# Kernel tuning notes

Hardware: AMD Instinct MI355X
Metric: run time of the kernel (lower is better)

Reference implementation:

```python
import jax, jax.numpy as jnp
import numpy as np

B, V, E, D_IN, D_OUT = 8, 10000, 160000, 128, 128
BN_EPS = 1e-5


def setup_inputs() -> dict:
    key = jax.random.key(0)
    ks = jax.random.split(key, 8)
    X = jax.random.normal(ks[0], (B, V, D_IN), dtype=jnp.float32)
    edge_attr = jax.random.normal(ks[1], (B, E), dtype=jnp.float32)
    W_node = jax.random.normal(ks[2], (D_OUT, D_IN), dtype=jnp.float32) * (1.0 / np.sqrt(D_IN))
    W_edge = jax.random.normal(ks[3], (D_OUT, 1), dtype=jnp.float32)
    W_self = jax.random.normal(ks[4], (D_OUT, D_IN), dtype=jnp.float32) * (1.0 / np.sqrt(D_IN))
    b_self = jax.random.normal(ks[5], (D_OUT,), dtype=jnp.float32) * 0.01
    gamma = jnp.ones((D_OUT,), dtype=jnp.float32)
    beta = jnp.zeros((D_OUT,), dtype=jnp.float32)
    edge_index = jax.random.randint(ks[6], (E, 2), 0, V, dtype=jnp.int32)
    return {"X": X, "edge_attr": edge_attr, "W_node": W_node, "W_edge": W_edge,
            "W_self": W_self, "b_self": b_self, "gamma": gamma, "beta": beta,
            "edge_index": edge_index}


def reference(X, edge_attr, W_node, W_edge, W_self, b_self, gamma, beta, edge_index):
    src = edge_index[:, 0]  # [E]
    dst = edge_index[:, 1]  # [E]
    # self-loop linear
    H = jnp.einsum('bvf,of->bvo', X, W_self) + b_self  # [B,V,D_OUT]
    # fused gather -> per-edge message -> scatter-add
    msg = jnp.einsum('bef,of->beo', X[:, src, :], W_node)  # [B,E,D_OUT]
    msg = msg + edge_attr[:, :, None] * W_edge[:, 0][None, None, :]
    aggregated = jnp.zeros_like(H).at[:, dst, :].add(msg)
    H = H + aggregated
    # BatchNorm1d over channel dim (training mode, biased variance over B*V)
    mean = jnp.mean(H, axis=(0, 1))
    var = jnp.var(H, axis=(0, 1))
    Hn = (H - mean) * jax.lax.rsqrt(var + BN_EPS) * gamma + beta
    return jax.nn.relu(Hn)
```

## Files before the change

### kernel.cpp

```cpp
#include <hip/hip_runtime.h>

#define B_ 8
#define V_ 10000
#define E_ 160000
#define DIN 128
#define DOUT 128
#define M_ (B_*V_)
#define NINV (1.0f/80000.0f)
#define BN_EPS 1e-5f

#define WS_COUNTS  0
#define WS_SUM     10000
#define WS_SUMSQ   10128
#define WS_ROWPTR  10512
#define WS_CURSOR  20513
#define WS_SSRC    30513
#define WS_SEID    190513
#define WS_S       350513
#define WS_WPK     430516
#define WS_XBF     446900
#define WS_ABF     5566900
#define WS_ZERO_UNITS 10256

typedef __attribute__((ext_vector_type(8))) short short8;
typedef __attribute__((ext_vector_type(4))) float f32x4;

__device__ inline unsigned short f2bf(float x) {
    union { float f; unsigned u; } v; v.f = x;
    unsigned r = v.u + 0x7FFFu + ((v.u >> 16) & 1u);
    return (unsigned short)(r >> 16);
}
__device__ inline float bf2f(unsigned short u) {
    union { unsigned u; float f; } v; v.u = ((unsigned)u) << 16;
    return v.f;
}

__global__ __launch_bounds__(256) void prep_kernel(
    const float* __restrict__ X, unsigned short* __restrict__ Xbf,
    const float* __restrict__ Wself, const float* __restrict__ Wnode,
    unsigned short* __restrict__ Wpk,
    const int* __restrict__ EI, int* __restrict__ counts)
{
    const int blk = blockIdx.x;
    const int t = threadIdx.x;
    if (blk < 10000) {
        int idx = blk * 256 + t;
        float4 v = ((const float4*)X)[idx];
        ushort4 o;
        o.x = f2bf(v.x); o.y = f2bf(v.y); o.z = f2bf(v.z); o.w = f2bf(v.w);
        ((ushort4*)Xbf)[idx] = o;
    } else if (blk < 10016) {
        int g = (blk - 10000) * 256 + t;
        int pair = g >> 6;
        int lane = g & 63;
        int ks = pair >> 3;
        int nt = pair & 7;
        int o = nt * 16 + (lane & 15);
        int k = ks * 32 + (lane >> 4) * 8;
        const float* wsrc = (k < 128) ? (Wself + o * 128 + k)
                                      : (Wnode + o * 128 + (k - 128));
        unsigned short* dst = Wpk + ((size_t)pair * 64 + lane) * 8;
#pragma unroll
        for (int j = 0; j < 8; ++j) dst[j] = f2bf(wsrc[j]);
    } else {
        int e = (blk - 10016) * 256 + t;
        if (e < E_) atomicAdd(&counts[EI[2 * e + 1]], 1);
    }
}

__global__ __launch_bounds__(256) void scan_kernel(
    const int* __restrict__ counts, int* __restrict__ row_ptr,
    int* __restrict__ cursor)
{
    __shared__ int psum[256];
    const int t = threadIdx.x;
    const int base = t * 40;
    int local[40];
    int s = 0;
#pragma unroll
    for (int i = 0; i < 40; ++i) {
        int idx = base + i;
        int c = (idx < V_) ? counts[idx] : 0;
        local[i] = s;
        s += c;
    }
    psum[t] = s;
    __syncthreads();
    for (int off = 1; off < 256; off <<= 1) {
        int v = (t >= off) ? psum[t - off] : 0;
        __syncthreads();
        psum[t] += v;
        __syncthreads();
    }
    int excl = (t == 0) ? 0 : psum[t - 1];
#pragma unroll
    for (int i = 0; i < 40; ++i) {
        int idx = base + i;
        if (idx < V_) {
            int rp = excl + local[i];
            row_ptr[idx] = rp;
            cursor[idx] = rp;
        }
    }
    if (t == 255) row_ptr[V_] = psum[255];
}

__global__ __launch_bounds__(256) void bucket_kernel(
    const int* __restrict__ EI, int* __restrict__ cursor,
    int* __restrict__ ssrc, int* __restrict__ seid)
{
    int e = blockIdx.x * 256 + threadIdx.x;
    if (e < E_) {
        int src = EI[2 * e];
        int dst = EI[2 * e + 1];
        int p = atomicAdd(&cursor[dst], 1);
        ssrc[p] = src;
        seid[p] = e;
    }
}

__global__ __launch_bounds__(256) void gather_kernel(
    const unsigned short* __restrict__ Xbf, const float* __restrict__ EA,
    const int* __restrict__ row_ptr, const int* __restrict__ ssrc,
    const int* __restrict__ seid, unsigned short* __restrict__ Abf,
    float* __restrict__ S)
{
    const int b = blockIdx.x & 7;
    const int dblk = blockIdx.x >> 3;
    const int w = threadIdx.x >> 6;
    const int lane = threadIdx.x & 63;
    const int d = dblk * 4 + w;
    const int wid = b * V_ + d;
    const int k0 = row_ptr[d];
    const int k1 = row_ptr[d + 1];
    const unsigned short* Xb = Xbf + (size_t)b * V_ * DIN + lane * 2;
    const float* EAb = EA + (size_t)b * E_;
    float ax = 0.0f, ay = 0.0f;
    float ea = 0.0f;
    for (int kb = k0; kb < k1; kb += 64) {
        int cnt = min(64, k1 - kb);
        int msrc = 0;
        if (lane < cnt) {
            msrc = ssrc[kb + lane];
            ea += EAb[seid[kb + lane]];
        }
        int j = 0;
        for (; j + 4 <= cnt; j += 4) {
            int s0 = __shfl(msrc, j);
            int s1 = __shfl(msrc, j + 1);
            int s2 = __shfl(msrc, j + 2);
            int s3 = __shfl(msrc, j + 3);
            ushort2 v0 = *(const ushort2*)(Xb + (size_t)s0 * DIN);
            ushort2 v1 = *(const ushort2*)(Xb + (size_t)s1 * DIN);
            ushort2 v2 = *(const ushort2*)(Xb + (size_t)s2 * DIN);
            ushort2 v3 = *(const ushort2*)(Xb + (size_t)s3 * DIN);
            ax += bf2f(v0.x) + bf2f(v1.x) + bf2f(v2.x) + bf2f(v3.x);
            ay += bf2f(v0.y) + bf2f(v1.y) + bf2f(v2.y) + bf2f(v3.y);
        }
        for (; j < cnt; ++j) {
            int s = __shfl(msrc, j);
            ushort2 v = *(const ushort2*)(Xb + (size_t)s * DIN);
            ax += bf2f(v.x); ay += bf2f(v.y);
        }
    }
    for (int off = 32; off; off >>= 1) ea += __shfl_down(ea, off);
    if (lane == 0) S[wid] = ea;
    ushort2 o;
    o.x = f2bf(ax); o.y = f2bf(ay);
    *(ushort2*)(Abf + (size_t)wid * DIN + lane * 2) = o;
}

__global__ __launch_bounds__(256) void mfma_gemm_kernel(
    const unsigned short* __restrict__ Xbf, const unsigned short* __restrict__ Abf,
    const unsigned short* __restrict__ Wpk, const float* __restrict__ S,
    const float* __restrict__ bself, const float* __restrict__ wedge,
    float* __restrict__ H, float* __restrict__ gsum, float* __restrict__ gsumsq)
{
    __shared__ float cs[128];
    __shared__ float css[128];
    const int t = threadIdx.x;
    const int wave = t >> 6;
    const int lane = t & 63;
    const int quad = lane >> 4;
    const int ln = lane & 15;
    const int rowbase = blockIdx.x * 128 + wave * 32;
    const int m0 = rowbase + ln;
    const int m1 = rowbase + 16 + ln;

    if (t < 128) { cs[t] = 0.0f; css[t] = 0.0f; }

    f32x4 acc[2][8];
#pragma unroll
    for (int mt = 0; mt < 2; ++mt)
#pragma unroll
        for (int nt = 0; nt < 8; ++nt) acc[mt][nt] = (f32x4){0.f, 0.f, 0.f, 0.f};

    const short* X0 = (const short*)Xbf + (size_t)m0 * DIN + quad * 8;
    const short* X1 = (const short*)Xbf + (size_t)m1 * DIN + quad * 8;
    const short* A0 = (const short*)Abf + (size_t)m0 * DIN + quad * 8;
    const short* A1 = (const short*)Abf + (size_t)m1 * DIN + quad * 8;
    const short* Wl = (const short*)Wpk + lane * 8;

#pragma unroll
    for (int ks = 0; ks < 8; ++ks) {
        short8 bfr[8];
#pragma unroll
        for (int nt = 0; nt < 8; ++nt)
            bfr[nt] = *(const short8*)(Wl + (size_t)(ks * 8 + nt) * 512);
        short8 af0, af1;
        if (ks < 4) {
            af0 = *(const short8*)(X0 + ks * 32);
            af1 = *(const short8*)(X1 + ks * 32);
        } else {
            af0 = *(const short8*)(A0 + (ks - 4) * 32);
            af1 = *(const short8*)(A1 + (ks - 4) * 32);
        }
#pragma unroll
        for (int nt = 0; nt < 8; ++nt) {
            acc[0][nt] = __builtin_amdgcn_mfma_f32_16x16x32_bf16(af0, bfr[nt], acc[0][nt], 0, 0, 0);
            acc[1][nt] = __builtin_amdgcn_mfma_f32_16x16x32_bf16(af1, bfr[nt], acc[1][nt], 0, 0, 0);
        }
    }

    float bs[8], we[8];
#pragma unroll
    for (int nt = 0; nt < 8; ++nt) {
        int c = nt * 16 + ln;
        bs[nt] = bself[c];
        we[nt] = wedge[c];
    }
    float psum[8], psq[8];
#pragma unroll
    for (int nt = 0; nt < 8; ++nt) { psum[nt] = 0.0f; psq[nt] = 0.0f; }

#pragma unroll
    for (int mt = 0; mt < 2; ++mt) {
        const int rbase = rowbase + mt * 16 + quad * 4;
        float sv[4];
#pragma unroll
        for (int r = 0; r < 4; ++r) sv[r] = S[rbase + r];
#pragma unroll
        for (int r = 0; r < 4; ++r) {
            float* Hr = H + (size_t)(rbase + r) * DOUT + ln;
#pragma unroll
            for (int nt = 0; nt < 8; ++nt) {
                float h = acc[mt][nt][r] + bs[nt] + sv[r] * we[nt];
                Hr[nt * 16] = h;
                psum[nt] += h;
                psq[nt] += h * h;
            }
        }
    }
#pragma unroll
    for (int nt = 0; nt < 8; ++nt) {
        psum[nt] += __shfl_down(psum[nt], 32);
        psum[nt] += __shfl_down(psum[nt], 16);
        psq[nt] += __shfl_down(psq[nt], 32);
        psq[nt] += __shfl_down(psq[nt], 16);
    }
    __syncthreads();
    if (lane < 16) {
#pragma unroll
        for (int nt = 0; nt < 8; ++nt) {
            atomicAdd(&cs[nt * 16 + ln], psum[nt]);
            atomicAdd(&css[nt * 16 + ln], psq[nt]);
        }
    }
    __syncthreads();
    if (t < 128) {
        atomicAdd(&gsum[t], cs[t]);
        atomicAdd(&gsumsq[t], css[t]);
    }
}

__global__ __launch_bounds__(256) void norm_relu_kernel(
    float* __restrict__ H, const float* __restrict__ gsum,
    const float* __restrict__ gsumsq, const float* __restrict__ gamma,
    const float* __restrict__ beta)
{
    int idx = blockIdx.x * 256 + threadIdx.x;
    int o4 = (idx & 31) * 4;
    float4 s = *(const float4*)(gsum + o4);
    float4 q = *(const float4*)(gsumsq + o4);
    float4 g = *(const float4*)(gamma + o4);
    float4 bt = *(const float4*)(beta + o4);
    float4 sc, sh;
    {
        float m0 = s.x * NINV, m1 = s.y * NINV, m2 = s.z * NINV, m3 = s.w * NINV;
        float r0 = rsqrtf(q.x * NINV - m0 * m0 + BN_EPS);
        float r1 = rsqrtf(q.y * NINV - m1 * m1 + BN_EPS);
        float r2 = rsqrtf(q.z * NINV - m2 * m2 + BN_EPS);
        float r3 = rsqrtf(q.w * NINV - m3 * m3 + BN_EPS);
        sc.x = g.x * r0; sc.y = g.y * r1; sc.z = g.z * r2; sc.w = g.w * r3;
        sh.x = bt.x - m0 * sc.x; sh.y = bt.y - m1 * sc.y;
        sh.z = bt.z - m2 * sc.z; sh.w = bt.w - m3 * sc.w;
    }
    float4 h = ((const float4*)H)[idx];
    h.x = fmaxf(h.x * sc.x + sh.x, 0.0f);
    h.y = fmaxf(h.y * sc.y + sh.y, 0.0f);
    h.z = fmaxf(h.z * sc.z + sh.z, 0.0f);
    h.w = fmaxf(h.w * sc.w + sh.w, 0.0f);
    ((float4*)H)[idx] = h;
}

extern "C" void kernel_launch(void* const* d_in, const int* in_sizes, int n_in,
                              void* d_out, int out_size, void* d_ws, size_t ws_size,
                              hipStream_t stream)
{
    const float* X      = (const float*)d_in[0];
    const float* EA     = (const float*)d_in[1];
    const float* Wnode  = (const float*)d_in[2];
    const float* Wedge  = (const float*)d_in[3];
    const float* Wself  = (const float*)d_in[4];
    const float* bself  = (const float*)d_in[5];
    const float* gamma  = (const float*)d_in[6];
    const float* beta   = (const float*)d_in[7];
    const int*   EI     = (const int*)d_in[8];

    int*   wsI    = (int*)d_ws;
    float* wsF    = (float*)d_ws;
    int*   counts = wsI + WS_COUNTS;
    float* gsum   = wsF + WS_SUM;
    float* gsumsq = wsF + WS_SUMSQ;
    int*   rowptr = wsI + WS_ROWPTR;
    int*   cursor = wsI + WS_CURSOR;
    int*   ssrc   = wsI + WS_SSRC;
    int*   seid   = wsI + WS_SEID;
    float* S      = wsF + WS_S;
    unsigned short* Wpk = (unsigned short*)(wsI + WS_WPK);
    unsigned short* Xbf = (unsigned short*)(wsI + WS_XBF);
    unsigned short* Abf = (unsigned short*)(wsI + WS_ABF);
    float* H      = (float*)d_out;

    hipMemsetAsync(d_ws, 0, (size_t)WS_ZERO_UNITS * 4, stream);

    prep_kernel<<<10641, 256, 0, stream>>>(X, Xbf, Wself, Wnode, Wpk, EI, counts);
    scan_kernel<<<1, 256, 0, stream>>>(counts, rowptr, cursor);
    bucket_kernel<<<(E_ + 255) / 256, 256, 0, stream>>>(EI, cursor, ssrc, seid);

    gather_kernel<<<M_ / 4, 256, 0, stream>>>(Xbf, EA, rowptr, ssrc, seid, Abf, S);

    mfma_gemm_kernel<<<M_ / 128, 256, 0, stream>>>(Xbf, Abf, Wpk, S, bself, Wedge,
                                                   H, gsum, gsumsq);

    norm_relu_kernel<<<(M_ * DOUT / 4) / 256, 256, 0, stream>>>(H, gsum, gsumsq,
                                                                gamma, beta);
}
```

Baseline: 235.7 us.

## Switch intermediates to fp16 and gather two edges per wave iteration

```diff
diff --git a/kernel.cpp b/kernel.cpp
--- a/kernel.cpp
+++ b/kernel.cpp
@@ -18,27 +18,26 @@
 #define WS_SEID    190513
 #define WS_S       350513
 #define WS_WPK     430516
-#define WS_XBF     446900
-#define WS_ABF     5566900
+#define WS_XH      446900
+#define WS_AH      5566900
 #define WS_ZERO_UNITS 10256
 
-typedef __attribute__((ext_vector_type(8))) short short8;
+typedef __attribute__((ext_vector_type(2))) _Float16 half2_t;
+typedef __attribute__((ext_vector_type(4))) _Float16 half4_t;
+typedef __attribute__((ext_vector_type(8))) _Float16 half8_t;
 typedef __attribute__((ext_vector_type(4))) float f32x4;
 
-__device__ inline unsigned short f2bf(float x) {
-    union { float f; unsigned u; } v; v.f = x;
-    unsigned r = v.u + 0x7FFFu + ((v.u >> 16) & 1u);
-    return (unsigned short)(r >> 16);
-}
-__device__ inline float bf2f(unsigned short u) {
-    union { unsigned u; float f; } v; v.u = ((unsigned)u) << 16;
-    return v.f;
+__device__ inline half2_t i2h(unsigned i) {
+    half2_t h; __builtin_memcpy(&h, &i, 4); return h;
+}
+__device__ inline unsigned h2i(half2_t h) {
+    unsigned i; __builtin_memcpy(&i, &h, 4); return i;
 }
 
 __global__ __launch_bounds__(256) void prep_kernel(
-    const float* __restrict__ X, unsigned short* __restrict__ Xbf,
+    const float* __restrict__ X, _Float16* __restrict__ Xh,
     const float* __restrict__ Wself, const float* __restrict__ Wnode,
-    unsigned short* __restrict__ Wpk,
+    _Float16* __restrict__ Wpk,
     const int* __restrict__ EI, int* __restrict__ counts)
 {
     const int blk = blockIdx.x;
@@ -46,9 +45,8 @@
     if (blk < 10000) {
         int idx = blk * 256 + t;
         float4 v = ((const float4*)X)[idx];
-        ushort4 o;
-        o.x = f2bf(v.x); o.y = f2bf(v.y); o.z = f2bf(v.z); o.w = f2bf(v.w);
-        ((ushort4*)Xbf)[idx] = o;
+        half4_t o = { (_Float16)v.x, (_Float16)v.y, (_Float16)v.z, (_Float16)v.w };
+        ((half4_t*)Xh)[idx] = o;
     } else if (blk < 10016) {
         int g = (blk - 10000) * 256 + t;
         int pair = g >> 6;
@@ -59,9 +57,9 @@
         int k = ks * 32 + (lane >> 4) * 8;
         const float* wsrc = (k < 128) ? (Wself + o * 128 + k)
                                       : (Wnode + o * 128 + (k - 128));
-        unsigned short* dst = Wpk + ((size_t)pair * 64 + lane) * 8;
-#pragma unroll
-        for (int j = 0; j < 8; ++j) dst[j] = f2bf(wsrc[j]);
+        _Float16* dst = Wpk + ((size_t)pair * 64 + lane) * 8;
+#pragma unroll
+        for (int j = 0; j < 8; ++j) dst[j] = (_Float16)wsrc[j];
     } else {
         int e = (blk - 10016) * 256 + t;
         if (e < E_) atomicAdd(&counts[EI[2 * e + 1]], 1);
@@ -120,22 +118,24 @@
 }
 
 __global__ __launch_bounds__(256) void gather_kernel(
-    const unsigned short* __restrict__ Xbf, const float* __restrict__ EA,
+    const _Float16* __restrict__ Xh, const float* __restrict__ EA,
     const int* __restrict__ row_ptr, const int* __restrict__ ssrc,
-    const int* __restrict__ seid, unsigned short* __restrict__ Abf,
+    const int* __restrict__ seid, _Float16* __restrict__ Ah,
     float* __restrict__ S)
 {
     const int b = blockIdx.x & 7;
     const int dblk = blockIdx.x >> 3;
     const int w = threadIdx.x >> 6;
     const int lane = threadIdx.x & 63;
+    const int half = lane >> 5;
+    const int sl = lane & 31;
     const int d = dblk * 4 + w;
     const int wid = b * V_ + d;
     const int k0 = row_ptr[d];
     const int k1 = row_ptr[d + 1];
-    const unsigned short* Xb = Xbf + (size_t)b * V_ * DIN + lane * 2;
+    const _Float16* Xb = Xh + (size_t)b * V_ * DIN + sl * 4;
     const float* EAb = EA + (size_t)b * E_;
-    float ax = 0.0f, ay = 0.0f;
+    half2_t a0 = (half2_t)0, a1 = (half2_t)0;
     float ea = 0.0f;
     for (int kb = k0; kb < k1; kb += 64) {
         int cnt = min(64, k1 - kb);
@@ -145,34 +145,47 @@
             ea += EAb[seid[kb + lane]];
         }
         int j = 0;
-        for (; j + 4 <= cnt; j += 4) {
-            int s0 = __shfl(msrc, j);
-            int s1 = __shfl(msrc, j + 1);
-            int s2 = __shfl(msrc, j + 2);
-            int s3 = __shfl(msrc, j + 3);
-            ushort2 v0 = *(const ushort2*)(Xb + (size_t)s0 * DIN);
-            ushort2 v1 = *(const ushort2*)(Xb + (size_t)s1 * DIN);
-            ushort2 v2 = *(const ushort2*)(Xb + (size_t)s2 * DIN);
-            ushort2 v3 = *(const ushort2*)(Xb + (size_t)s3 * DIN);
-            ax += bf2f(v0.x) + bf2f(v1.x) + bf2f(v2.x) + bf2f(v3.x);
-            ay += bf2f(v0.y) + bf2f(v1.y) + bf2f(v2.y) + bf2f(v3.y);
-        }
-        for (; j < cnt; ++j) {
+        for (; j + 8 <= cnt; j += 8) {
+#pragma unroll
+            for (int u = 0; u < 4; ++u) {
+                int s = __shfl(msrc, j + u * 2 + half);
+                uint2 v = *(const uint2*)(Xb + (size_t)s * DIN);
+                a0 += i2h(v.x);
+                a1 += i2h(v.y);
+            }
+        }
+        for (; j + 2 <= cnt; j += 2) {
+            int s = __shfl(msrc, j + half);
+            uint2 v = *(const uint2*)(Xb + (size_t)s * DIN);
+            a0 += i2h(v.x);
+            a1 += i2h(v.y);
+        }
+        if (j < cnt) {
             int s = __shfl(msrc, j);
-            ushort2 v = *(const ushort2*)(Xb + (size_t)s * DIN);
-            ax += bf2f(v.x); ay += bf2f(v.y);
-        }
-    }
+            if (half == 0) {
+                uint2 v = *(const uint2*)(Xb + (size_t)s * DIN);
+                a0 += i2h(v.x);
+                a1 += i2h(v.y);
+            }
+        }
+    }
+    unsigned c0 = __shfl_down(h2i(a0), 32);
+    unsigned c1 = __shfl_down(h2i(a1), 32);
+    a0 += i2h(c0);
+    a1 += i2h(c1);
     for (int off = 32; off; off >>= 1) ea += __shfl_down(ea, off);
     if (lane == 0) S[wid] = ea;
-    ushort2 o;
-    o.x = f2bf(ax); o.y = f2bf(ay);
-    *(ushort2*)(Abf + (size_t)wid * DIN + lane * 2) = o;
+    if (half == 0) {
+        uint2 o;
+        o.x = h2i(a0);
+        o.y = h2i(a1);
+        *(uint2*)(Ah + (size_t)wid * DIN + sl * 4) = o;
+    }
 }
 
 __global__ __launch_bounds__(256) void mfma_gemm_kernel(
-    const unsigned short* __restrict__ Xbf, const unsigned short* __restrict__ Abf,
-    const unsigned short* __restrict__ Wpk, const float* __restrict__ S,
+    const _Float16* __restrict__ Xh, const _Float16* __restrict__ Ah,
+    const _Float16* __restrict__ Wpk, const float* __restrict__ S,
     const float* __restrict__ bself, const float* __restrict__ wedge,
     float* __restrict__ H, float* __restrict__ gsum, float* __restrict__ gsumsq)
 {
@@ -195,30 +208,30 @@
 #pragma unroll
         for (int nt = 0; nt < 8; ++nt) acc[mt][nt] = (f32x4){0.f, 0.f, 0.f, 0.f};
 
-    const short* X0 = (const short*)Xbf + (size_t)m0 * DIN + quad * 8;
-    const short* X1 = (const short*)Xbf + (size_t)m1 * DIN + quad * 8;
-    const short* A0 = (const short*)Abf + (size_t)m0 * DIN + quad * 8;
-    const short* A1 = (const short*)Abf + (size_t)m1 * DIN + quad * 8;
-    const short* Wl = (const short*)Wpk + lane * 8;
+    const _Float16* X0 = Xh + (size_t)m0 * DIN + quad * 8;
+    const _Float16* X1 = Xh + (size_t)m1 * DIN + quad * 8;
+    const _Float16* A0 = Ah + (size_t)m0 * DIN + quad * 8;
+    const _Float16* A1 = Ah + (size_t)m1 * DIN + quad * 8;
+    const _Float16* Wl = Wpk + lane * 8;
 
 #pragma unroll
     for (int ks = 0; ks < 8; ++ks) {
-        short8 bfr[8];
+        half8_t bfr[8];
 #pragma unroll
         for (int nt = 0; nt < 8; ++nt)
-            bfr[nt] = *(const short8*)(Wl + (size_t)(ks * 8 + nt) * 512);
-        short8 af0, af1;
+            bfr[nt] = *(const half8_t*)(Wl + (size_t)(ks * 8 + nt) * 512);
+        half8_t af0, af1;
         if (ks < 4) {
-            af0 = *(const short8*)(X0 + ks * 32);
-            af1 = *(const short8*)(X1 + ks * 32);
+            af0 = *(const half8_t*)(X0 + ks * 32);
+            af1 = *(const half8_t*)(X1 + ks * 32);
         } else {
-            af0 = *(const short8*)(A0 + (ks - 4) * 32);
-            af1 = *(const short8*)(A1 + (ks - 4) * 32);
+            af0 = *(const half8_t*)(A0 + (ks - 4) * 32);
+            af1 = *(const half8_t*)(A1 + (ks - 4) * 32);
         }
 #pragma unroll
         for (int nt = 0; nt < 8; ++nt) {
-            acc[0][nt] = __builtin_amdgcn_mfma_f32_16x16x32_bf16(af0, bfr[nt], acc[0][nt], 0, 0, 0);
-            acc[1][nt] = __builtin_amdgcn_mfma_f32_16x16x32_bf16(af1, bfr[nt], acc[1][nt], 0, 0, 0);
+            acc[0][nt] = __builtin_amdgcn_mfma_f32_16x16x32_f16(af0, bfr[nt], acc[0][nt], 0, 0, 0);
+            acc[1][nt] = __builtin_amdgcn_mfma_f32_16x16x32_f16(af1, bfr[nt], acc[1][nt], 0, 0, 0);
         }
     }
 
@@ -327,20 +340,20 @@
     int*   ssrc   = wsI + WS_SSRC;
     int*   seid   = wsI + WS_SEID;
     float* S      = wsF + WS_S;
-    unsigned short* Wpk = (unsigned short*)(wsI + WS_WPK);
-    unsigned short* Xbf = (unsigned short*)(wsI + WS_XBF);
-    unsigned short* Abf = (unsigned short*)(wsI + WS_ABF);
+    _Float16* Wpk = (_Float16*)(wsI + WS_WPK);
+    _Float16* Xh  = (_Float16*)(wsI + WS_XH);
+    _Float16* Ah  = (_Float16*)(wsI + WS_AH);
     float* H      = (float*)d_out;
 
     hipMemsetAsync(d_ws, 0, (size_t)WS_ZERO_UNITS * 4, stream);
 
-    prep_kernel<<<10641, 256, 0, stream>>>(X, Xbf, Wself, Wnode, Wpk, EI, counts);
+    prep_kernel<<<10641, 256, 0, stream>>>(X, Xh, Wself, Wnode, Wpk, EI, counts);
     scan_kernel<<<1, 256, 0, stream>>>(counts, rowptr, cursor);
     bucket_kernel<<<(E_ + 255) / 256, 256, 0, stream>>>(EI, cursor, ssrc, seid);
 
-    gather_kernel<<<M_ / 4, 256, 0, stream>>>(Xbf, EA, rowptr, ssrc, seid, Abf, S);
-
-    mfma_gemm_kernel<<<M_ / 128, 256, 0, stream>>>(Xbf, Abf, Wpk, S, bself, Wedge,
+    gather_kernel<<<M_ / 4, 256, 0, stream>>>(Xh, EA, rowptr, ssrc, seid, Ah, S);
+
+    mfma_gemm_kernel<<<M_ / 128, 256, 0, stream>>>(Xh, Ah, Wpk, S, bself, Wedge,
                                                    H, gsum, gsumsq);
 
     norm_relu_kernel<<<(M_ * DOUT / 4) / 256, 256, 0, stream>>>(H, gsum, gsumsq,
```

Result: no change. 233.3 us (-1.0%).
